# Optimization experiments

Hardware: AMD Instinct MI355X
Metric: run time of the kernel (lower is better)

Reference implementation:

```python
import jax, jax.numpy as jnp
import numpy as np
from jax import lax

SEQ_LEN = 131072
EMBED_DIM = 256
DT = 0.1
EPS = 1e-8


def setup_inputs() -> dict:
    key = jax.random.key(0)
    k1, k2, k3, k4 = jax.random.split(key, 4)
    psi_real = jax.random.normal(k1, (SEQ_LEN, EMBED_DIM), dtype=jnp.float32)
    psi_imag = jax.random.normal(k2, (SEQ_LEN, EMBED_DIM), dtype=jnp.float32)
    # Hermitian Hamiltonian: H = (A + A^H)/2 with A ~ 0.1*randn (complex)
    a_re = jax.random.normal(k3, (EMBED_DIM, EMBED_DIM), dtype=jnp.float32) * 0.1
    a_im = jax.random.normal(k4, (EMBED_DIM, EMBED_DIM), dtype=jnp.float32) * 0.1
    ham_real = (a_re + a_re.T) / 2.0   # symmetric real part
    ham_imag = (a_im - a_im.T) / 2.0   # antisymmetric imag part
    hbar = jnp.ones((1,), dtype=jnp.float32)
    return {"psi_real": psi_real, "psi_imag": psi_imag,
            "ham_real": ham_real, "ham_imag": ham_imag,
            "hbar": hbar, "time_steps": 10}


def reference(psi_real, psi_imag, ham_real, ham_imag, hbar, time_steps):
    psi = psi_real + 1j * psi_imag                      # [S, D] complex64
    H = ham_real + 1j * ham_imag                        # [D, D] complex64
    coef = (-1j / hbar[0].astype(jnp.complex64)) * DT   # scalar complex

    def step(p, _):
        h_psi = p @ H.T                                 # [S, D] complex matmul
        p = p + coef * h_psi                            # Schrodinger Euler step
        norms = jnp.sqrt(jnp.sum(p.real * p.real + p.imag * p.imag,
                                 axis=1, keepdims=True))  # torch.norm over dim=1
        return p / (norms + EPS), None

    psi_out, _ = lax.scan(step, psi, None, length=time_steps)
    return psi_out
```

## Files before the change

### kernel.cpp

```cpp
#include <hip/hip_runtime.h>

#define SEQ 131072
#define DIM 256
#define DTC 0.1f
#define EPSC 1e-8f

typedef __attribute__((ext_vector_type(8))) short bf16x8;
typedef __attribute__((ext_vector_type(4))) float f32x4;
typedef __attribute__((ext_vector_type(4))) int   i32x4;

static __device__ __forceinline__ unsigned short f2bf(float f){
  unsigned int u = __builtin_bit_cast(unsigned int, f);
  u += 0x7fffu + ((u >> 16) & 1u);
  return (unsigned short)(u >> 16);
}

__global__ __launch_bounds__(1024)
void k_chain1(const float* __restrict__ hr, const float* __restrict__ hi,
              const float* __restrict__ hbar, const int* __restrict__ ts,
              float* __restrict__ m1r, float* __restrict__ m1i,
              float* __restrict__ outr, float* __restrict__ outi)
{
  __shared__ float rowr[256], rowi[256];
  __shared__ float pr_[4][256], pi_[4][256];
  const int tid = threadIdx.x, c = tid & 255, q = tid >> 8;
  const int r = blockIdx.x;
  const float s = DTC / hbar[0];
  const int T = ts[0];
  const bool b4 = ((T >> 4) & 1) != 0;
  const bool b3 = ((T >> 3) & 1) != 0;

  float m1rc = 0.f, m1ic = 0.f;
  if (q == 0){
    const int idx = r*256 + c;
    const float diag = (r == c) ? 1.0f : 0.0f;
    m1rc = diag + s * hi[idx];
    m1ic =       -s * hr[idx];
    m1r[idx] = m1rc;  m1i[idx] = m1ic;
  }

  if (!b4){
    if (q == 0){
      const float diag = (r == c) ? 1.0f : 0.0f;
      outr[r*256+c] = b3 ? m1rc : diag;
      outi[r*256+c] = b3 ? m1ic : 0.0f;
    }
    return;
  }

  if (q == 0){ rowr[c] = m1rc; rowi[c] = m1ic; }
  __syncthreads();
  float ar = 0.f, ai = 0.f;
  const int k0 = q * 64;
  #pragma unroll 4
  for (int k = k0; k < k0 + 64; ++k){
    const int idx = k*256 + c;
    const float diag = (k == c) ? 1.0f : 0.0f;
    const float br = diag + s * hi[idx];
    const float bi =       -s * hr[idx];
    const float xr = rowr[k], xi = rowi[k];
    ar = fmaf(xr, br, fmaf(-xi, bi, ar));
    ai = fmaf(xr, bi, fmaf( xi, br, ai));
  }
  pr_[q][c] = ar; pi_[q][c] = ai;
  __syncthreads();

  if (!b3){
    if (q == 0){
      outr[r*256+c] = pr_[0][c]+pr_[1][c]+pr_[2][c]+pr_[3][c];
      outi[r*256+c] = pi_[0][c]+pi_[1][c]+pi_[2][c]+pi_[3][c];
    }
    return;
  }
  if (q == 0){
    rowr[c] = pr_[0][c]+pr_[1][c]+pr_[2][c]+pr_[3][c];
    rowi[c] = pi_[0][c]+pi_[1][c]+pi_[2][c]+pi_[3][c];
  }
  __syncthreads();
  ar = 0.f; ai = 0.f;
  #pragma unroll 4
  for (int k = k0; k < k0 + 64; ++k){
    const int idx = k*256 + c;
    const float diag = (k == c) ? 1.0f : 0.0f;
    const float br = diag + s * hi[idx];
    const float bi =       -s * hr[idx];
    const float xr = rowr[k], xi = rowi[k];
    ar = fmaf(xr, br, fmaf(-xi, bi, ar));
    ai = fmaf(xr, bi, fmaf( xi, br, ai));
  }
  pr_[q][c] = ar; pi_[q][c] = ai;
  __syncthreads();
  if (q == 0){
    outr[r*256+c] = pr_[0][c]+pr_[1][c]+pr_[2][c]+pr_[3][c];
    outi[r*256+c] = pi_[0][c]+pi_[1][c]+pi_[2][c]+pi_[3][c];
  }
}

template<int BIT>
__global__ __launch_bounds__(1024)
void k_step2(const float* __restrict__ inr, const float* __restrict__ ini,
             const float* __restrict__ m1r, const float* __restrict__ m1i,
             const int* __restrict__ ts,
             float* __restrict__ outr, float* __restrict__ outi)
{
  __shared__ float rr[256], ri[256];
  __shared__ float pr_[4][256], pi_[4][256];
  const int tid = threadIdx.x, c = tid & 255, q = tid >> 8;
  const int r = blockIdx.x;
  if (q == 0){ rr[c] = inr[r*256 + c]; ri[c] = ini[r*256 + c]; }
  __syncthreads();

  float ar = 0.f, ai = 0.f;
  const int k0 = q * 64;
  #pragma unroll 8
  for (int k = k0; k < k0 + 64; ++k){
    const float br = inr[k*256 + c], bi = ini[k*256 + c];
    const float xr = rr[k],          xi = ri[k];
    ar = fmaf(xr, br, fmaf(-xi, bi, ar));
    ai = fmaf(xr, bi, fmaf( xi, br, ai));
  }
  pr_[q][c] = ar; pi_[q][c] = ai;
  __syncthreads();

  const bool bit = ((ts[0] >> BIT) & 1) != 0;
  if (!bit){
    if (q == 0){
      outr[r*256+c] = pr_[0][c]+pr_[1][c]+pr_[2][c]+pr_[3][c];
      outi[r*256+c] = pi_[0][c]+pi_[1][c]+pi_[2][c]+pi_[3][c];
    }
    return;
  }
  if (q == 0){
    rr[c] = pr_[0][c]+pr_[1][c]+pr_[2][c]+pr_[3][c];
    ri[c] = pi_[0][c]+pi_[1][c]+pi_[2][c]+pi_[3][c];
  }
  __syncthreads();
  ar = 0.f; ai = 0.f;
  #pragma unroll 8
  for (int k = k0; k < k0 + 64; ++k){
    const float br = m1r[k*256 + c], bi = m1i[k*256 + c];
    const float xr = rr[k],          xi = ri[k];
    ar = fmaf(xr, br, fmaf(-xi, bi, ar));
    ai = fmaf(xr, bi, fmaf( xi, br, ai));
  }
  pr_[q][c] = ar; pi_[q][c] = ai;
  __syncthreads();
  if (q == 0){
    outr[r*256+c] = pr_[0][c]+pr_[1][c]+pr_[2][c]+pr_[3][c];
    outi[r*256+c] = pi_[0][c]+pi_[1][c]+pi_[2][c]+pi_[3][c];
  }
}

__global__ __launch_bounds__(1024)
void k_last2(const float* __restrict__ inr, const float* __restrict__ ini,
             const float* __restrict__ m1r, const float* __restrict__ m1i,
             const int* __restrict__ ts,
             float* __restrict__ outr, float* __restrict__ outi,
             unsigned short* __restrict__ fragbuf)
{
  __shared__ float rr[256], ri[256];
  __shared__ float pr_[4][256], pi_[4][256];
  const int tid = threadIdx.x, c = tid & 255, q = tid >> 8;
  const int r = blockIdx.x;
  if (q == 0){ rr[c] = inr[r*256 + c]; ri[c] = ini[r*256 + c]; }
  __syncthreads();

  float ar = 0.f, ai = 0.f;
  const int k0 = q * 64;
  #pragma unroll 8
  for (int k = k0; k < k0 + 64; ++k){
    const float br = inr[k*256 + c], bi = ini[k*256 + c];
    const float xr = rr[k],          xi = ri[k];
    ar = fmaf(xr, br, fmaf(-xi, bi, ar));
    ai = fmaf(xr, bi, fmaf( xi, br, ai));
  }
  pr_[q][c] = ar; pi_[q][c] = ai;
  __syncthreads();

  const bool bit = (ts[0] & 1) != 0;
  if (bit){
    if (q == 0){
      rr[c] = pr_[0][c]+pr_[1][c]+pr_[2][c]+pr_[3][c];
      ri[c] = pi_[0][c]+pi_[1][c]+pi_[2][c]+pi_[3][c];
    }
    __syncthreads();
    ar = 0.f; ai = 0.f;
    #pragma unroll 8
    for (int k = k0; k < k0 + 64; ++k){
      const float br = m1r[k*256 + c], bi = m1i[k*256 + c];
      const float xr = rr[k],          xi = ri[k];
      ar = fmaf(xr, br, fmaf(-xi, bi, ar));
      ai = fmaf(xr, bi, fmaf( xi, br, ai));
    }
    pr_[q][c] = ar; pi_[q][c] = ai;
    __syncthreads();
  }

  if (q == 0){
    const float orr = pr_[0][c]+pr_[1][c]+pr_[2][c]+pr_[3][c];
    const float oii = pi_[0][c]+pi_[1][c]+pi_[2][c]+pi_[3][c];
    outr[r*256+c] = orr;
    outi[r*256+c] = oii;
    if (fragbuf){
      const int C = r, K = c;
      const int ftid = (C>>5)*64 + ((K>>3)&3)*16 + (C&15);
      const int fid  = (((C>>4)&1)*8 + (K>>5))*2;
      fragbuf[((size_t)fid*512     + ftid)*8 + (K&7)] = f2bf(orr - ((r==c)?1.0f:0.0f));
      fragbuf[((size_t)(fid+1)*512 + ftid)*8 + (K&7)] = f2bf(oii);
    }
  }
}

template<int STORE_COMPLEX>
__global__ __launch_bounds__(512, 6)
void apply7(const float* __restrict__ psi_re, const float* __restrict__ psi_im,
            const unsigned short* __restrict__ fragbuf,
            const int* __restrict__ tsteps, float* __restrict__ out)
{
  __shared__ alignas(16) unsigned short a_re[32][272];
  __shared__ alignas(16) unsigned short a_im[32][272];
  __shared__ float partials[32][8];

  const int tid  = threadIdx.x;
  const int wv   = tid >> 6;
  const int lane = tid & 63;
  const int lq   = lane >> 4;
  const int lr   = lane & 15;
  const int brow = blockIdx.x << 5;
  const int cbase = wv << 5;
  const int T = tsteps[0];
  const bf16x8* fb = reinterpret_cast<const bf16x8*>(fragbuf);

  const int srow  = tid >> 4;
  const int scol0 = (tid & 15) << 4;
  {
    const float4* p4 = reinterpret_cast<const float4*>(&psi_re[(size_t)(brow + srow)*DIM + scol0]);
    const float4 v0 = p4[0], v1 = p4[1], v2 = p4[2], v3 = p4[3];
    bf16x8 p0, p1;
    p0[0]=(short)f2bf(v0.x); p0[1]=(short)f2bf(v0.y); p0[2]=(short)f2bf(v0.z); p0[3]=(short)f2bf(v0.w);
    p0[4]=(short)f2bf(v1.x); p0[5]=(short)f2bf(v1.y); p0[6]=(short)f2bf(v1.z); p0[7]=(short)f2bf(v1.w);
    p1[0]=(short)f2bf(v2.x); p1[1]=(short)f2bf(v2.y); p1[2]=(short)f2bf(v2.z); p1[3]=(short)f2bf(v2.w);
    p1[4]=(short)f2bf(v3.x); p1[5]=(short)f2bf(v3.y); p1[6]=(short)f2bf(v3.z); p1[7]=(short)f2bf(v3.w);
    *reinterpret_cast<bf16x8*>(&a_re[srow][scol0])     = p0;
    *reinterpret_cast<bf16x8*>(&a_re[srow][scol0 + 8]) = p1;
  }
  {
    const float4* p4 = reinterpret_cast<const float4*>(&psi_im[(size_t)(brow + srow)*DIM + scol0]);
    const float4 v0 = p4[0], v1 = p4[1], v2 = p4[2], v3 = p4[3];
    bf16x8 p0, p1;
    p0[0]=(short)f2bf(v0.x); p0[1]=(short)f2bf(v0.y); p0[2]=(short)f2bf(v0.z); p0[3]=(short)f2bf(v0.w);
    p0[4]=(short)f2bf(v1.x); p0[5]=(short)f2bf(v1.y); p0[6]=(short)f2bf(v1.z); p0[7]=(short)f2bf(v1.w);
    p1[0]=(short)f2bf(v2.x); p1[1]=(short)f2bf(v2.y); p1[2]=(short)f2bf(v2.z); p1[3]=(short)f2bf(v2.w);
    p1[4]=(short)f2bf(v3.x); p1[5]=(short)f2bf(v3.y); p1[6]=(short)f2bf(v3.z); p1[7]=(short)f2bf(v3.w);
    *reinterpret_cast<bf16x8*>(&a_im[srow][scol0])     = p0;
    *reinterpret_cast<bf16x8*>(&a_im[srow][scol0 + 8]) = p1;
  }
  __syncthreads();

  float gre[2][2][4], gim[2][2][4];
  #pragma unroll
  for (int ct = 0; ct < 2; ++ct){
    f32x4 accr[2], acci[2];
    accr[0] = (f32x4){0.f,0.f,0.f,0.f}; accr[1] = (f32x4){0.f,0.f,0.f,0.f};
    acci[0] = (f32x4){0.f,0.f,0.f,0.f}; acci[1] = (f32x4){0.f,0.f,0.f,0.f};
    #pragma unroll
    for (int kt = 0; kt < 8; ++kt){
      const bf16x8 br = fb[((ct*8 + kt)*2 + 0)*512 + tid];
      const bf16x8 bi = fb[((ct*8 + kt)*2 + 1)*512 + tid];
      #pragma unroll
      for (int rt = 0; rt < 2; ++rt){
        const bf16x8 apr = *reinterpret_cast<const bf16x8*>(&a_re[rt*16 + lr][kt*32 + lq*8]);
        const bf16x8 api = *reinterpret_cast<const bf16x8*>(&a_im[rt*16 + lr][kt*32 + lq*8]);
        const i32x4 tneg = __builtin_bit_cast(i32x4, api) ^ (i32x4)(int)0x80008000;
        const bf16x8 apin = __builtin_bit_cast(bf16x8, tneg);
        accr[rt] = __builtin_amdgcn_mfma_f32_16x16x32_bf16(apr,  br, accr[rt], 0,0,0);
        accr[rt] = __builtin_amdgcn_mfma_f32_16x16x32_bf16(apin, bi, accr[rt], 0,0,0);
        acci[rt] = __builtin_amdgcn_mfma_f32_16x16x32_bf16(apr,  bi, acci[rt], 0,0,0);
        acci[rt] = __builtin_amdgcn_mfma_f32_16x16x32_bf16(api,  br, acci[rt], 0,0,0);
      }
    }
    #pragma unroll
    for (int rt = 0; rt < 2; ++rt)
      #pragma unroll
      for (int j = 0; j < 4; ++j){
        gre[rt][ct][j] = accr[rt][j];
        gim[rt][ct][j] = acci[rt][j];
      }
  }

  #pragma unroll
  for (int rt = 0; rt < 2; ++rt)
    #pragma unroll
    for (int ct = 0; ct < 2; ++ct)
      #pragma unroll
      for (int j = 0; j < 4; ++j){
        const size_t off = (size_t)(brow + rt*16 + lq*4 + j)*DIM + cbase + ct*16 + lr;
        gre[rt][ct][j] += psi_re[off];
        gim[rt][ct][j] += psi_im[off];
      }

  #pragma unroll
  for (int rt = 0; rt < 2; ++rt)
    #pragma unroll
    for (int j = 0; j < 4; ++j){
      float v = gre[rt][0][j]*gre[rt][0][j] + gim[rt][0][j]*gim[rt][0][j]
              + gre[rt][1][j]*gre[rt][1][j] + gim[rt][1][j]*gim[rt][1][j];
      v += __shfl_xor(v, 1);
      v += __shfl_xor(v, 2);
      v += __shfl_xor(v, 4);
      v += __shfl_xor(v, 8);
      if (lr == 0) partials[rt*16 + lq*4 + j][wv] = v;
    }
  __syncthreads();

  #pragma unroll
  for (int rt = 0; rt < 2; ++rt)
    #pragma unroll
    for (int j = 0; j < 4; ++j){
      const int rl = rt*16 + lq*4 + j;
      const f32x4 p0 = *reinterpret_cast<const f32x4*>(&partials[rl][0]);
      const f32x4 p1 = *reinterpret_cast<const f32x4*>(&partials[rl][4]);
      const float nrm = ((p0[0]+p0[1]) + (p0[2]+p0[3]))
                      + ((p1[0]+p1[1]) + (p1[2]+p1[3]));
      const float sc = (T == 0) ? 1.0f : 1.0f/(sqrtf(nrm) + EPSC);
      const size_t off = (size_t)(brow + rl)*DIM + cbase + lr;
      if (STORE_COMPLEX){
        float2 v0 = {gre[rt][0][j]*sc, gim[rt][0][j]*sc};
        float2 v1 = {gre[rt][1][j]*sc, gim[rt][1][j]*sc};
        *reinterpret_cast<float2*>(&out[off*2])      = v0;
        *reinterpret_cast<float2*>(&out[(off+16)*2]) = v1;
      } else {
        out[off]    = gre[rt][0][j]*sc;
        out[off+16] = gre[rt][1][j]*sc;
      }
    }
}

template<int STORE_COMPLEX>
__global__ __launch_bounds__(512, 2)
void apply_kernel(const float* __restrict__ psi_re, const float* __restrict__ psi_im,
                  const float* __restrict__ Pre,    const float* __restrict__ Pim,
                  const int* __restrict__ tsteps,   float* __restrict__ out)
{
  __shared__ alignas(16) unsigned short a_re[64][272];
  __shared__ alignas(16) unsigned short a_im[64][272];
  __shared__ float partials[64][8];
  __shared__ float scales[64];

  const int tid  = threadIdx.x;
  const int wv   = tid >> 6;
  const int lane = tid & 63;
  const int lq   = lane >> 4;
  const int lr   = lane & 15;
  const int brow = blockIdx.x << 6;
  const int cbase = wv << 5;
  const int T = tsteps[0];

  bf16x8 bhr[2][8], bhi[2][8];
  #pragma unroll
  for (int ct = 0; ct < 2; ++ct){
    const int c = cbase + ct*16 + lr;
    #pragma unroll
    for (int kt = 0; kt < 8; ++kt){
      const int kb = kt*32 + lq*8;
      const float4 pr0 = *reinterpret_cast<const float4*>(&Pre[c*DIM + kb]);
      const float4 pr1 = *reinterpret_cast<const float4*>(&Pre[c*DIM + kb + 4]);
      const float4 pi0 = *reinterpret_cast<const float4*>(&Pim[c*DIM + kb]);
      const float4 pi1 = *reinterpret_cast<const float4*>(&Pim[c*DIM + kb + 4]);
      const float re8[8] = {pr0.x,pr0.y,pr0.z,pr0.w, pr1.x,pr1.y,pr1.z,pr1.w};
      const float im8[8] = {pi0.x,pi0.y,pi0.z,pi0.w, pi1.x,pi1.y,pi1.z,pi1.w};
      bf16x8 vr, vi;
      #pragma unroll
      for (int i = 0; i < 8; ++i){
        const float rv = re8[i] - ((c == kb + i) ? 1.0f : 0.0f);
        vr[i] = (short)f2bf(rv);
        vi[i] = (short)f2bf(im8[i]);
      }
      bhr[ct][kt] = vr; bhi[ct][kt] = vi;
    }
  }

  float sre[4][2][4], simg[4][2][4];
  #pragma unroll
  for (int rt = 0; rt < 4; ++rt)
    #pragma unroll
    for (int ct = 0; ct < 2; ++ct)
      #pragma unroll
      for (int j = 0; j < 4; ++j){
        const int row = brow + rt*16 + lq*4 + j;
        const int col = cbase + ct*16 + lr;
        const float xr = psi_re[row*DIM + col];
        const float xi = psi_im[row*DIM + col];
        sre [rt][ct][j] = xr;
        simg[rt][ct][j] = xi;
        a_re[rt*16 + lq*4 + j][col] = f2bf(xr);
        a_im[rt*16 + lq*4 + j][col] = f2bf(xi);
      }
  __syncthreads();

  #pragma unroll
  for (int rt = 0; rt < 4; ++rt){
    f32x4 ar0 = {0.f,0.f,0.f,0.f}, ar1 = {0.f,0.f,0.f,0.f};
    f32x4 ai0 = {0.f,0.f,0.f,0.f}, ai1 = {0.f,0.f,0.f,0.f};
    #pragma unroll
    for (int kt = 0; kt < 8; ++kt){
      const int arow = rt*16 + lr;
      const int kofs = kt*32 + lq*8;
      bf16x8 apr = *reinterpret_cast<const bf16x8*>(&a_re[arow][kofs]);
      bf16x8 api = *reinterpret_cast<const bf16x8*>(&a_im[arow][kofs]);
      i32x4 tneg = __builtin_bit_cast(i32x4, api) ^ (i32x4)(int)0x80008000;
      bf16x8 apin = __builtin_bit_cast(bf16x8, tneg);
      ar0 = __builtin_amdgcn_mfma_f32_16x16x32_bf16(apr,  bhr[0][kt], ar0, 0,0,0);
      ai0 = __builtin_amdgcn_mfma_f32_16x16x32_bf16(apr,  bhi[0][kt], ai0, 0,0,0);
      ar1 = __builtin_amdgcn_mfma_f32_16x16x32_bf16(apr,  bhr[1][kt], ar1, 0,0,0);
      ai1 = __builtin_amdgcn_mfma_f32_16x16x32_bf16(apr,  bhi[1][kt], ai1, 0,0,0);
      ar0 = __builtin_amdgcn_mfma_f32_16x16x32_bf16(apin, bhi[0][kt], ar0, 0,0,0);
      ai0 = __builtin_amdgcn_mfma_f32_16x16x32_bf16(api,  bhr[0][kt], ai0, 0,0,0);
      ar1 = __builtin_amdgcn_mfma_f32_16x16x32_bf16(apin, bhi[1][kt], ar1, 0,0,0);
      ai1 = __builtin_amdgcn_mfma_f32_16x16x32_bf16(api,  bhr[1][kt], ai1, 0,0,0);
    }
    float ss[4];
    #pragma unroll
    for (int j = 0; j < 4; ++j){
      sre [rt][0][j] += ar0[j];
      simg[rt][0][j] += ai0[j];
      sre [rt][1][j] += ar1[j];
      simg[rt][1][j] += ai1[j];
      float v = sre[rt][0][j]*sre[rt][0][j] + simg[rt][0][j]*simg[rt][0][j]
              + sre[rt][1][j]*sre[rt][1][j] + simg[rt][1][j]*simg[rt][1][j];
      v += __shfl_xor(v, 1);
      v += __shfl_xor(v, 2);
      v += __shfl_xor(v, 4);
      v += __shfl_xor(v, 8);
      ss[j] = v;
    }
    if (lr == 0){
      #pragma unroll
      for (int j = 0; j < 4; ++j)
        partials[rt*16 + lq*4 + j][wv] = ss[j];
    }
  }
  __syncthreads();

  if (tid < 64){
    float acc = 0.f;
    #pragma unroll
    for (int w = 0; w < 8; ++w) acc += partials[tid][w];
    scales[tid] = (T == 0) ? 1.0f : 1.0f / (sqrtf(acc) + EPSC);
  }
  __syncthreads();

  #pragma unroll
  for (int rt = 0; rt < 4; ++rt)
    #pragma unroll
    for (int ct = 0; ct < 2; ++ct)
      #pragma unroll
      for (int j = 0; j < 4; ++j){
        const int row = brow + rt*16 + lq*4 + j;
        const int col = cbase + ct*16 + lr;
        const float sc = scales[rt*16 + lq*4 + j];
        const float xr = sre [rt][ct][j] * sc;
        const float xi = simg[rt][ct][j] * sc;
        if (STORE_COMPLEX){
          float2 v2 = {xr, xi};
          *reinterpret_cast<float2*>(&out[(size_t)(row*DIM + col)*2]) = v2;
        } else {
          out[row*DIM + col] = xr;
        }
      }
}

template<int STORE_COMPLEX>
__global__ __launch_bounds__(512, 2)
void qevolve_kernel(const float* __restrict__ psi_re, const float* __restrict__ psi_im,
                    const float* __restrict__ ham_re, const float* __restrict__ ham_im,
                    const float* __restrict__ hbar,   const int* __restrict__ tsteps,
                    float* __restrict__ out)
{
  __shared__ alignas(16) unsigned short a_re[64][272];
  __shared__ alignas(16) unsigned short a_im[64][272];
  __shared__ float partials[64][8];
  __shared__ float scales[64];

  const int tid  = threadIdx.x;
  const int wv   = tid >> 6;
  const int lane = tid & 63;
  const int lq   = lane >> 4;
  const int lr   = lane & 15;
  const int brow = blockIdx.x << 6;
  const int cbase = wv << 5;
  const float cs = DTC / hbar[0];
  const int T = tsteps[0];

  bf16x8 bhr[2][8], bhi[2][8];
  #pragma unroll
  for (int ct = 0; ct < 2; ++ct){
    const int c = cbase + ct*16 + lr;
    #pragma unroll
    for (int kt = 0; kt < 8; ++kt){
      const int kb = kt*32 + lq*8;
      bf16x8 vr, vi;
      #pragma unroll
      for (int i = 0; i < 8; ++i){
        vr[i] = (short)f2bf(ham_re[c*DIM + kb + i]);
        vi[i] = (short)f2bf(ham_im[c*DIM + kb + i]);
      }
      bhr[ct][kt] = vr; bhi[ct][kt] = vi;
    }
  }

  float sre[4][2][4], simg[4][2][4];
  #pragma unroll
  for (int rt = 0; rt < 4; ++rt)
    #pragma unroll
    for (int ct = 0; ct < 2; ++ct)
      #pragma unroll
      for (int j = 0; j < 4; ++j){
        const int row = brow + rt*16 + lq*4 + j;
        const int col = cbase + ct*16 + lr;
        sre [rt][ct][j] = psi_re[row*DIM + col];
        simg[rt][ct][j] = psi_im[row*DIM + col];
      }

  for (int s = 0; s < T; ++s){
    #pragma unroll
    for (int rt = 0; rt < 4; ++rt)
      #pragma unroll
      for (int ct = 0; ct < 2; ++ct)
        #pragma unroll
        for (int j = 0; j < 4; ++j){
          const int row = rt*16 + lq*4 + j;
          const int col = cbase + ct*16 + lr;
          a_re[row][col] = f2bf(sre [rt][ct][j]);
          a_im[row][col] = f2bf(simg[rt][ct][j]);
        }
    __syncthreads();

    #pragma unroll
    for (int rt = 0; rt < 4; ++rt){
      f32x4 ar0 = {0.f,0.f,0.f,0.f}, ar1 = {0.f,0.f,0.f,0.f};
      f32x4 ai0 = {0.f,0.f,0.f,0.f}, ai1 = {0.f,0.f,0.f,0.f};
      #pragma unroll
      for (int kt = 0; kt < 8; ++kt){
        const int arow = rt*16 + lr;
        const int kofs = kt*32 + lq*8;
        bf16x8 apr = *reinterpret_cast<const bf16x8*>(&a_re[arow][kofs]);
        bf16x8 api = *reinterpret_cast<const bf16x8*>(&a_im[arow][kofs]);
        i32x4 tneg = __builtin_bit_cast(i32x4, api) ^ (i32x4)(int)0x80008000;
        bf16x8 apin = __builtin_bit_cast(bf16x8, tneg);
        ar0 = __builtin_amdgcn_mfma_f32_16x16x32_bf16(apr,  bhr[0][kt], ar0, 0,0,0);
        ai0 = __builtin_amdgcn_mfma_f32_16x16x32_bf16(apr,  bhi[0][kt], ai0, 0,0,0);
        ar1 = __builtin_amdgcn_mfma_f32_16x16x32_bf16(apr,  bhr[1][kt], ar1, 0,0,0);
        ai1 = __builtin_amdgcn_mfma_f32_16x16x32_bf16(apr,  bhi[1][kt], ai1, 0,0,0);
        ar0 = __builtin_amdgcn_mfma_f32_16x16x32_bf16(apin, bhi[0][kt], ar0, 0,0,0);
        ai0 = __builtin_amdgcn_mfma_f32_16x16x32_bf16(api,  bhr[0][kt], ai0, 0,0,0);
        ar1 = __builtin_amdgcn_mfma_f32_16x16x32_bf16(apin, bhi[1][kt], ar1, 0,0,0);
        ai1 = __builtin_amdgcn_mfma_f32_16x16x32_bf16(api,  bhr[1][kt], ai1, 0,0,0);
      }
      float ss[4];
      #pragma unroll
      for (int j = 0; j < 4; ++j){
        sre [rt][0][j] += cs * ai0[j];
        simg[rt][0][j] -= cs * ar0[j];
        sre [rt][1][j] += cs * ai1[j];
        simg[rt][1][j] -= cs * ar1[j];
        float v = sre[rt][0][j]*sre[rt][0][j] + simg[rt][0][j]*simg[rt][0][j]
                + sre[rt][1][j]*sre[rt][1][j] + simg[rt][1][j]*simg[rt][1][j];
        v += __shfl_xor(v, 1);
        v += __shfl_xor(v, 2);
        v += __shfl_xor(v, 4);
        v += __shfl_xor(v, 8);
        ss[j] = v;
      }
      if (lr == 0){
        #pragma unroll
        for (int j = 0; j < 4; ++j)
          partials[rt*16 + lq*4 + j][wv] = ss[j];
      }
    }
    __syncthreads();

    if (tid < 64){
      float acc = 0.f;
      #pragma unroll
      for (int w = 0; w < 8; ++w) acc += partials[tid][w];
      scales[tid] = 1.0f / (sqrtf(acc) + EPSC);
    }
    __syncthreads();

    #pragma unroll
    for (int rt = 0; rt < 4; ++rt)
      #pragma unroll
      for (int j = 0; j < 4; ++j){
        const float sc = scales[rt*16 + lq*4 + j];
        sre [rt][0][j] *= sc; sre [rt][1][j] *= sc;
        simg[rt][0][j] *= sc; simg[rt][1][j] *= sc;
      }
  }

  #pragma unroll
  for (int rt = 0; rt < 4; ++rt)
    #pragma unroll
    for (int ct = 0; ct < 2; ++ct)
      #pragma unroll
      for (int j = 0; j < 4; ++j){
        const int row = brow + rt*16 + lq*4 + j;
        const int col = cbase + ct*16 + lr;
        if (STORE_COMPLEX){
          out[(size_t)(row*DIM + col)*2 + 0] = sre [rt][ct][j];
          out[(size_t)(row*DIM + col)*2 + 1] = simg[rt][ct][j];
        } else {
          out[row*DIM + col] = sre[rt][ct][j];
        }
      }
}

extern "C" void kernel_launch(void* const* d_in, const int* in_sizes, int n_in,
                              void* d_out, int out_size, void* d_ws, size_t ws_size,
                              hipStream_t stream)
{
  const float* psi_re = (const float*)d_in[0];
  const float* psi_im = (const float*)d_in[1];
  const float* ham_re = (const float*)d_in[2];
  const float* ham_im = (const float*)d_in[3];
  const float* hbar   = (const float*)d_in[4];
  const int*   tstep  = (const int*)d_in[5];
  float* out = (float*)d_out;

  const size_t NMAT    = (size_t)DIM * DIM;
  const size_t WS_MAT  = 6 * NMAT * sizeof(float);
  const size_t WS_FRAG = 2 * 8 * 2 * 512 * 16;

  const bool cplx = (out_size == 2 * SEQ * DIM);

  if (d_ws != nullptr && ws_size >= WS_MAT){
    float* w   = (float*)d_ws;
    float* m1r = w + 0*NMAT; float* m1i = w + 1*NMAT;
    float* Ar  = w + 2*NMAT; float* Ai  = w + 3*NMAT;
    float* Br  = w + 4*NMAT; float* Bi  = w + 5*NMAT;
    const bool have_frag = (ws_size >= WS_MAT + WS_FRAG);
    unsigned short* fragbuf = have_frag ? (unsigned short*)(w + 6*NMAT) : nullptr;

    k_chain1  <<<256, 1024, 0, stream>>>(ham_re, ham_im, hbar, tstep, m1r, m1i, Br, Bi);
    k_step2<2><<<256, 1024, 0, stream>>>(Br, Bi, m1r, m1i, tstep, Ar, Ai);
    k_step2<1><<<256, 1024, 0, stream>>>(Ar, Ai, m1r, m1i, tstep, Br, Bi);
    k_last2   <<<256, 1024, 0, stream>>>(Br, Bi, m1r, m1i, tstep, Ar, Ai, fragbuf);

    if (have_frag){
      dim3 grid(SEQ / 32), block(512);
      if (cplx)
        apply7<1><<<grid, block, 0, stream>>>(psi_re, psi_im, fragbuf, tstep, out);
      else
        apply7<0><<<grid, block, 0, stream>>>(psi_re, psi_im, fragbuf, tstep, out);
    } else {
      dim3 grid(SEQ / 64), block(512);
      if (cplx)
        apply_kernel<1><<<grid, block, 0, stream>>>(psi_re, psi_im, Ar, Ai, tstep, out);
      else
        apply_kernel<0><<<grid, block, 0, stream>>>(psi_re, psi_im, Ar, Ai, tstep, out);
    }
  } else {
    dim3 grid(SEQ / 64), block(512);
    if (cplx)
      qevolve_kernel<1><<<grid, block, 0, stream>>>(psi_re, psi_im, ham_re, ham_im, hbar, tstep, out);
    else
      qevolve_kernel<0><<<grid, block, 0, stream>>>(psi_re, psi_im, ham_re, ham_im, hbar, tstep, out);
  }

  (void)in_sizes; (void)n_in;
}
```

Before: 209.7 us.

## Shrink apply tile to 16 rows and reuse split bf16 psi from LDS for residual

```diff
diff --git a/kernel.cpp b/kernel.cpp
--- a/kernel.cpp
+++ b/kernel.cpp
@@ -13,6 +13,10 @@
   unsigned int u = __builtin_bit_cast(unsigned int, f);
   u += 0x7fffu + ((u >> 16) & 1u);
   return (unsigned short)(u >> 16);
+}
+static __device__ __forceinline__ float bf2f(unsigned short h){
+  unsigned int u = ((unsigned int)h) << 16;
+  return __builtin_bit_cast(float, u);
 }
 
 __global__ __launch_bounds__(1024)
@@ -212,128 +216,122 @@
 }
 
 template<int STORE_COMPLEX>
-__global__ __launch_bounds__(512, 6)
-void apply7(const float* __restrict__ psi_re, const float* __restrict__ psi_im,
+__global__ __launch_bounds__(512, 8)
+void apply8(const float* __restrict__ psi_re, const float* __restrict__ psi_im,
             const unsigned short* __restrict__ fragbuf,
             const int* __restrict__ tsteps, float* __restrict__ out)
 {
-  __shared__ alignas(16) unsigned short a_re[32][272];
-  __shared__ alignas(16) unsigned short a_im[32][272];
-  __shared__ float partials[32][8];
+  __shared__ alignas(16) unsigned short a_hi_re[16][272];
+  __shared__ alignas(16) unsigned short a_lo_re[16][272];
+  __shared__ alignas(16) unsigned short a_hi_im[16][272];
+  __shared__ alignas(16) unsigned short a_lo_im[16][272];
+  __shared__ float partials[16][8];
 
   const int tid  = threadIdx.x;
   const int wv   = tid >> 6;
   const int lane = tid & 63;
   const int lq   = lane >> 4;
   const int lr   = lane & 15;
-  const int brow = blockIdx.x << 5;
+  const int brow = blockIdx.x << 4;
   const int cbase = wv << 5;
   const int T = tsteps[0];
   const bf16x8* fb = reinterpret_cast<const bf16x8*>(fragbuf);
 
-  const int srow  = tid >> 4;
-  const int scol0 = (tid & 15) << 4;
+  const int srow  = tid >> 5;
+  const int scol0 = (tid & 31) << 3;
   {
     const float4* p4 = reinterpret_cast<const float4*>(&psi_re[(size_t)(brow + srow)*DIM + scol0]);
-    const float4 v0 = p4[0], v1 = p4[1], v2 = p4[2], v3 = p4[3];
-    bf16x8 p0, p1;
-    p0[0]=(short)f2bf(v0.x); p0[1]=(short)f2bf(v0.y); p0[2]=(short)f2bf(v0.z); p0[3]=(short)f2bf(v0.w);
-    p0[4]=(short)f2bf(v1.x); p0[5]=(short)f2bf(v1.y); p0[6]=(short)f2bf(v1.z); p0[7]=(short)f2bf(v1.w);
-    p1[0]=(short)f2bf(v2.x); p1[1]=(short)f2bf(v2.y); p1[2]=(short)f2bf(v2.z); p1[3]=(short)f2bf(v2.w);
-    p1[4]=(short)f2bf(v3.x); p1[5]=(short)f2bf(v3.y); p1[6]=(short)f2bf(v3.z); p1[7]=(short)f2bf(v3.w);
-    *reinterpret_cast<bf16x8*>(&a_re[srow][scol0])     = p0;
-    *reinterpret_cast<bf16x8*>(&a_re[srow][scol0 + 8]) = p1;
+    const float4 v0 = p4[0], v1 = p4[1];
+    const float q8[8] = {v0.x,v0.y,v0.z,v0.w, v1.x,v1.y,v1.z,v1.w};
+    bf16x8 hh, ll;
+    #pragma unroll
+    for (int i = 0; i < 8; ++i){
+      const unsigned short h = f2bf(q8[i]);
+      hh[i] = (short)h;
+      ll[i] = (short)f2bf(q8[i] - bf2f(h));
+    }
+    *reinterpret_cast<bf16x8*>(&a_hi_re[srow][scol0]) = hh;
+    *reinterpret_cast<bf16x8*>(&a_lo_re[srow][scol0]) = ll;
   }
   {
     const float4* p4 = reinterpret_cast<const float4*>(&psi_im[(size_t)(brow + srow)*DIM + scol0]);
-    const float4 v0 = p4[0], v1 = p4[1], v2 = p4[2], v3 = p4[3];
-    bf16x8 p0, p1;
-    p0[0]=(short)f2bf(v0.x); p0[1]=(short)f2bf(v0.y); p0[2]=(short)f2bf(v0.z); p0[3]=(short)f2bf(v0.w);
-    p0[4]=(short)f2bf(v1.x); p0[5]=(short)f2bf(v1.y); p0[6]=(short)f2bf(v1.z); p0[7]=(short)f2bf(v1.w);
-    p1[0]=(short)f2bf(v2.x); p1[1]=(short)f2bf(v2.y); p1[2]=(short)f2bf(v2.z); p1[3]=(short)f2bf(v2.w);
-    p1[4]=(short)f2bf(v3.x); p1[5]=(short)f2bf(v3.y); p1[6]=(short)f2bf(v3.z); p1[7]=(short)f2bf(v3.w);
-    *reinterpret_cast<bf16x8*>(&a_im[srow][scol0])     = p0;
-    *reinterpret_cast<bf16x8*>(&a_im[srow][scol0 + 8]) = p1;
-  }
-  __syncthreads();
-
-  float gre[2][2][4], gim[2][2][4];
+    const float4 v0 = p4[0], v1 = p4[1];
+    const float q8[8] = {v0.x,v0.y,v0.z,v0.w, v1.x,v1.y,v1.z,v1.w};
+    bf16x8 hh, ll;
+    #pragma unroll
+    for (int i = 0; i < 8; ++i){
+      const unsigned short h = f2bf(q8[i]);
+      hh[i] = (short)h;
+      ll[i] = (short)f2bf(q8[i] - bf2f(h));
+    }
+    *reinterpret_cast<bf16x8*>(&a_hi_im[srow][scol0]) = hh;
+    *reinterpret_cast<bf16x8*>(&a_lo_im[srow][scol0]) = ll;
+  }
+  __syncthreads();
+
+  float gre[2][4], gim[2][4];
   #pragma unroll
   for (int ct = 0; ct < 2; ++ct){
-    f32x4 accr[2], acci[2];
-    accr[0] = (f32x4){0.f,0.f,0.f,0.f}; accr[1] = (f32x4){0.f,0.f,0.f,0.f};
-    acci[0] = (f32x4){0.f,0.f,0.f,0.f}; acci[1] = (f32x4){0.f,0.f,0.f,0.f};
+    f32x4 accr = (f32x4){0.f,0.f,0.f,0.f};
+    f32x4 acci = (f32x4){0.f,0.f,0.f,0.f};
     #pragma unroll
     for (int kt = 0; kt < 8; ++kt){
       const bf16x8 br = fb[((ct*8 + kt)*2 + 0)*512 + tid];
       const bf16x8 bi = fb[((ct*8 + kt)*2 + 1)*512 + tid];
-      #pragma unroll
-      for (int rt = 0; rt < 2; ++rt){
-        const bf16x8 apr = *reinterpret_cast<const bf16x8*>(&a_re[rt*16 + lr][kt*32 + lq*8]);
-        const bf16x8 api = *reinterpret_cast<const bf16x8*>(&a_im[rt*16 + lr][kt*32 + lq*8]);
-        const i32x4 tneg = __builtin_bit_cast(i32x4, api) ^ (i32x4)(int)0x80008000;
-        const bf16x8 apin = __builtin_bit_cast(bf16x8, tneg);
-        accr[rt] = __builtin_amdgcn_mfma_f32_16x16x32_bf16(apr,  br, accr[rt], 0,0,0);
-        accr[rt] = __builtin_amdgcn_mfma_f32_16x16x32_bf16(apin, bi, accr[rt], 0,0,0);
-        acci[rt] = __builtin_amdgcn_mfma_f32_16x16x32_bf16(apr,  bi, acci[rt], 0,0,0);
-        acci[rt] = __builtin_amdgcn_mfma_f32_16x16x32_bf16(api,  br, acci[rt], 0,0,0);
-      }
-    }
-    #pragma unroll
-    for (int rt = 0; rt < 2; ++rt)
-      #pragma unroll
-      for (int j = 0; j < 4; ++j){
-        gre[rt][ct][j] = accr[rt][j];
-        gim[rt][ct][j] = acci[rt][j];
-      }
-  }
-
-  #pragma unroll
-  for (int rt = 0; rt < 2; ++rt)
-    #pragma unroll
-    for (int ct = 0; ct < 2; ++ct)
-      #pragma unroll
-      for (int j = 0; j < 4; ++j){
-        const size_t off = (size_t)(brow + rt*16 + lq*4 + j)*DIM + cbase + ct*16 + lr;
-        gre[rt][ct][j] += psi_re[off];
-        gim[rt][ct][j] += psi_im[off];
-      }
-
-  #pragma unroll
-  for (int rt = 0; rt < 2; ++rt)
+      const bf16x8 apr = *reinterpret_cast<const bf16x8*>(&a_hi_re[lr][kt*32 + lq*8]);
+      const bf16x8 api = *reinterpret_cast<const bf16x8*>(&a_hi_im[lr][kt*32 + lq*8]);
+      const i32x4 tneg = __builtin_bit_cast(i32x4, api) ^ (i32x4)(int)0x80008000;
+      const bf16x8 apin = __builtin_bit_cast(bf16x8, tneg);
+      accr = __builtin_amdgcn_mfma_f32_16x16x32_bf16(apr,  br, accr, 0,0,0);
+      accr = __builtin_amdgcn_mfma_f32_16x16x32_bf16(apin, bi, accr, 0,0,0);
+      acci = __builtin_amdgcn_mfma_f32_16x16x32_bf16(apr,  bi, acci, 0,0,0);
+      acci = __builtin_amdgcn_mfma_f32_16x16x32_bf16(api,  br, acci, 0,0,0);
+    }
+    #pragma unroll
+    for (int j = 0; j < 4; ++j){ gre[ct][j] = accr[j]; gim[ct][j] = acci[j]; }
+  }
+
+  #pragma unroll
+  for (int ct = 0; ct < 2; ++ct)
     #pragma unroll
     for (int j = 0; j < 4; ++j){
-      float v = gre[rt][0][j]*gre[rt][0][j] + gim[rt][0][j]*gim[rt][0][j]
-              + gre[rt][1][j]*gre[rt][1][j] + gim[rt][1][j]*gim[rt][1][j];
-      v += __shfl_xor(v, 1);
-      v += __shfl_xor(v, 2);
-      v += __shfl_xor(v, 4);
-      v += __shfl_xor(v, 8);
-      if (lr == 0) partials[rt*16 + lq*4 + j][wv] = v;
-    }
-  __syncthreads();
-
-  #pragma unroll
-  for (int rt = 0; rt < 2; ++rt)
-    #pragma unroll
-    for (int j = 0; j < 4; ++j){
-      const int rl = rt*16 + lq*4 + j;
-      const f32x4 p0 = *reinterpret_cast<const f32x4*>(&partials[rl][0]);
-      const f32x4 p1 = *reinterpret_cast<const f32x4*>(&partials[rl][4]);
-      const float nrm = ((p0[0]+p0[1]) + (p0[2]+p0[3]))
-                      + ((p1[0]+p1[1]) + (p1[2]+p1[3]));
-      const float sc = (T == 0) ? 1.0f : 1.0f/(sqrtf(nrm) + EPSC);
-      const size_t off = (size_t)(brow + rl)*DIM + cbase + lr;
-      if (STORE_COMPLEX){
-        float2 v0 = {gre[rt][0][j]*sc, gim[rt][0][j]*sc};
-        float2 v1 = {gre[rt][1][j]*sc, gim[rt][1][j]*sc};
-        *reinterpret_cast<float2*>(&out[off*2])      = v0;
-        *reinterpret_cast<float2*>(&out[(off+16)*2]) = v1;
-      } else {
-        out[off]    = gre[rt][0][j]*sc;
-        out[off+16] = gre[rt][1][j]*sc;
-      }
-    }
+      const int row = lq*4 + j;
+      const int col = cbase + ct*16 + lr;
+      gre[ct][j] += bf2f(a_hi_re[row][col]) + bf2f(a_lo_re[row][col]);
+      gim[ct][j] += bf2f(a_hi_im[row][col]) + bf2f(a_lo_im[row][col]);
+    }
+
+  #pragma unroll
+  for (int j = 0; j < 4; ++j){
+    float v = gre[0][j]*gre[0][j] + gim[0][j]*gim[0][j]
+            + gre[1][j]*gre[1][j] + gim[1][j]*gim[1][j];
+    v += __shfl_xor(v, 1);
+    v += __shfl_xor(v, 2);
+    v += __shfl_xor(v, 4);
+    v += __shfl_xor(v, 8);
+    if (lr == 0) partials[lq*4 + j][wv] = v;
+  }
+  __syncthreads();
+
+  #pragma unroll
+  for (int j = 0; j < 4; ++j){
+    const int rl = lq*4 + j;
+    const f32x4 p0 = *reinterpret_cast<const f32x4*>(&partials[rl][0]);
+    const f32x4 p1 = *reinterpret_cast<const f32x4*>(&partials[rl][4]);
+    const float nrm = ((p0[0]+p0[1]) + (p0[2]+p0[3]))
+                    + ((p1[0]+p1[1]) + (p1[2]+p1[3]));
+    const float sc = (T == 0) ? 1.0f : 1.0f/(sqrtf(nrm) + EPSC);
+    const size_t off = (size_t)(brow + rl)*DIM + cbase + lr;
+    if (STORE_COMPLEX){
+      float2 v0 = {gre[0][j]*sc, gim[0][j]*sc};
+      float2 v1 = {gre[1][j]*sc, gim[1][j]*sc};
+      *reinterpret_cast<float2*>(&out[off*2])      = v0;
+      *reinterpret_cast<float2*>(&out[(off+16)*2]) = v1;
+    } else {
+      out[off]    = gre[0][j]*sc;
+      out[off+16] = gre[1][j]*sc;
+    }
+  }
 }
 
 template<int STORE_COMPLEX>
@@ -647,11 +645,11 @@
     k_last2   <<<256, 1024, 0, stream>>>(Br, Bi, m1r, m1i, tstep, Ar, Ai, fragbuf);
 
     if (have_frag){
-      dim3 grid(SEQ / 32), block(512);
+      dim3 grid(SEQ / 16), block(512);
       if (cplx)
-        apply7<1><<<grid, block, 0, stream>>>(psi_re, psi_im, fragbuf, tstep, out);
+        apply8<1><<<grid, block, 0, stream>>>(psi_re, psi_im, fragbuf, tstep, out);
       else
-        apply7<0><<<grid, block, 0, stream>>>(psi_re, psi_im, fragbuf, tstep, out);
+        apply8<0><<<grid, block, 0, stream>>>(psi_re, psi_im, fragbuf, tstep, out);
     } else {
       dim3 grid(SEQ / 64), block(512);
       if (cplx)
```

Result: slower. 216.4 us (+3.2%).
